# Performance work log

Hardware: AMD Instinct MI355X
Metric: run time of the kernel (lower is better)

## Reference

```python
import jax, jax.numpy as jnp
import numpy as np

N = 65536
DIMS = [512, 1000, 500, 250, 1]


def setup_inputs() -> dict:
    key = jax.random.key(0)
    ks = jax.random.split(key, 7)

    def init_w(k, fan_in, fan_out):
        return (jax.random.normal(k, (fan_in, fan_out), jnp.float32)
                / np.float32(np.sqrt(fan_in)))

    return {
        "repr_xy_hat": jax.random.normal(ks[0], (N, DIMS[0]), jnp.float32),
        "repr_xy": jax.random.normal(ks[1], (N, DIMS[0]), jnp.float32),
        "W1": init_w(ks[2], DIMS[0], DIMS[1]), "b1": jnp.zeros((DIMS[1],), jnp.float32),
        "W2": init_w(ks[3], DIMS[1], DIMS[2]), "b2": jnp.zeros((DIMS[2],), jnp.float32),
        "W3": init_w(ks[4], DIMS[2], DIMS[3]), "b3": jnp.zeros((DIMS[3],), jnp.float32),
        "W4": init_w(ks[5], DIMS[3], DIMS[4]), "b4": jnp.zeros((DIMS[4],), jnp.float32),
    }


def _disc_logits(x, W1, b1, W2, b2, W3, b3, W4, b4):
    # Batched version of the per-sample Linear-ReLU chain; sigmoid is folded
    # into the numerically stable BCE losses below.
    h = jax.nn.relu(x @ W1 + b1)
    h = jax.nn.relu(h @ W2 + b2)
    h = jax.nn.relu(h @ W3 + b3)
    return (h @ W4 + b4)[:, 0]  # [N]


def reference(repr_xy_hat, repr_xy, W1, b1, W2, b2, W3, b3, W4, b4):
    z_fake = _disc_logits(repr_xy_hat, W1, b1, W2, b2, W3, b3, W4, b4)  # [N]
    z_real = _disc_logits(repr_xy, W1, b1, W2, b2, W3, b3, W4, b4)      # [N]
    # generator loss: sum_i -log sigmoid(z_fake_i) = softplus(-z_fake)
    loss_F = jnp.sum(jax.nn.softplus(-z_fake))
    # discriminator loss: sum_i [-log sigmoid(z_real_i) - log(1 - sigmoid(z_fake_i))]
    # pred is detached in the original -> stop_gradient on the fake logits.
    z_fake_d = jax.lax.stop_gradient(z_fake)
    loss_D = jnp.sum(jax.nn.softplus(-z_real) + jax.nn.softplus(z_fake_d))
    return (loss_F, loss_D)
```

## Files before the change

### kernel.cpp

```cpp
#include <hip/hip_runtime.h>
#include <hip/hip_bf16.h>
#include <cmath>

using short4v = __attribute__((ext_vector_type(4))) short;
using f32x16  = __attribute__((ext_vector_type(16))) float;
using int8v   = __attribute__((ext_vector_type(8))) int;

#define MFMASC(a,b,c) __builtin_amdgcn_mfma_scale_f32_32x32x64_f8f6f4( \
    a, b, c, 0, 0, 0, 0x7F7F7F7F, 0, 0x7F7F7F7F)

__device__ __forceinline__ unsigned short f2bf(float f) {
    union { float f; unsigned u; } v; v.f = f;
    unsigned u = v.u;
    return (unsigned short)((u + 0x7FFFu + ((u >> 16) & 1u)) >> 16);
}
__device__ __forceinline__ float bf2f(unsigned short h) {
    union { unsigned u; float f; } v; v.u = ((unsigned)h) << 16;
    return v.f;
}
__device__ __forceinline__ float softplus(float x) {
    return fmaxf(x, 0.f) + log1pf(expf(-fabsf(x)));
}
__device__ __forceinline__ unsigned f4_to_fp8x4(float a, float b, float c, float d) {
    int v = __builtin_amdgcn_cvt_pk_fp8_f32(a, b, 0, false);
    v = __builtin_amdgcn_cvt_pk_fp8_f32(c, d, v, true);
    return (unsigned)v;
}
__device__ __forceinline__ int8v ld_a(const unsigned char* base, int o0, int o1) {
    int8v r;
    *((uint4*)&r)     = *(const uint4*)(base + o0);
    *((uint4*)&r + 1) = *(const uint4*)(base + o1);
    return r;
}
__device__ __forceinline__ int8v ld_w(const uint4* p) {
    int8v r;
    *((uint4*)&r)     = p[0];
    *((uint4*)&r + 1) = p[1];
    return r;
}

__global__ void pack_w_fp8g(const float* __restrict__ W, uint4* __restrict__ out,
                            int K_real, int M_real, int KG, int CT) {
    int tid = blockIdx.x * blockDim.x + threadIdx.x;
    if (tid >= CT * KG * 64) return;
    int lane = tid & 63;
    int t    = tid >> 6;
    int kg   = t % KG;
    int ct   = t / KG;
    int m  = ct * 32 + (lane & 31);
    int kb = kg * 64 + ((lane >> 5) << 5);
    float f[32];
#pragma unroll
    for (int j = 0; j < 32; ++j) {
        int k = kb + j;
        f[j] = (k < K_real && m < M_real) ? W[(size_t)k * M_real + m] : 0.f;
    }
    uint4 o0, o1;
    o0.x = f4_to_fp8x4(f[0],  f[1],  f[2],  f[3]);
    o0.y = f4_to_fp8x4(f[4],  f[5],  f[6],  f[7]);
    o0.z = f4_to_fp8x4(f[8],  f[9],  f[10], f[11]);
    o0.w = f4_to_fp8x4(f[12], f[13], f[14], f[15]);
    o1.x = f4_to_fp8x4(f[16], f[17], f[18], f[19]);
    o1.y = f4_to_fp8x4(f[20], f[21], f[22], f[23]);
    o1.z = f4_to_fp8x4(f[24], f[25], f[26], f[27]);
    o1.w = f4_to_fp8x4(f[28], f[29], f[30], f[31]);
    out[(size_t)tid * 2]     = o0;
    out[(size_t)tid * 2 + 1] = o1;
}

__global__ void pack_bias(const float* __restrict__ b1, const float* __restrict__ b2,
                          const float* __restrict__ b3, float* __restrict__ out) {
    int i = blockIdx.x * 256 + threadIdx.x;
    if (i < 1024)      out[i] = (i < 1000) ? b1[i] : 0.f;
    else if (i < 1536) { int j = i - 1024; out[i] = (j < 500) ? b2[j] : 0.f; }
    else if (i < 1792) { int j = i - 1536; out[i] = (j < 250) ? b3[j] : 0.f; }
}

__global__ __launch_bounds__(512, 4) void fused_mlp(
    const float* __restrict__ Xf, const float* __restrict__ Xr,
    const uint4* __restrict__ pW1, const uint4* __restrict__ pW2,
    const uint4* __restrict__ pW3, const float* __restrict__ biasp,
    const float* __restrict__ W4, const float* __restrict__ b4,
    float* __restrict__ partials)
{
    __shared__ __align__(16) unsigned char smem[66048];
    float* red = (float*)(smem + 65536);

    const int tidx = threadIdx.x;
    const int wid  = tidx >> 6;
    const int lane = tidx & 63;
    const int l31  = lane & 31;
    const int hi   = lane >> 5;
    const int swz  = (l31 & 15) << 4;

    const long grow0 = (long)blockIdx.x * 64;
    const float* X = (grow0 < 65536) ? (Xf + (size_t)grow0 * 512)
                                     : (Xr + (size_t)(grow0 - 65536) * 512);

#pragma unroll 1
    for (int gb = 0; gb < 4; ++gb) {
        float4 xr[4];
#pragma unroll
        for (int it = 0; it < 4; ++it) {
            int idx = (gb * 4 + it) * 512 + tidx;
            int r = idx >> 7; int k0 = (idx & 127) * 4;
            xr[it] = *(const float4*)(X + (size_t)r * 512 + k0);
        }
#pragma unroll
        for (int it = 0; it < 4; ++it) {
            int idx = (gb * 4 + it) * 512 + tidx;
            int r = idx >> 7; int k0 = (idx & 127) * 4;
            int pos = 512 + ((k0 & 0x1F0) ^ ((r & 15) << 4)) + (k0 & 12);
            *(unsigned*)(smem + r * 1024 + pos) =
                f4_to_fp8x4(xr[it].x, xr[it].y, xr[it].z, xr[it].w);
        }
    }
    __syncthreads();

#pragma unroll 1
    for (int p = 0; p < 2; ++p) {
        const uint4* wpA = pW1 + ((size_t)((p * 16 + wid * 2 + 0) * 8) * 64 + lane) * 2;
        const uint4* wpB = pW1 + ((size_t)((p * 16 + wid * 2 + 1) * 8) * 64 + lane) * 2;
        f32x16 acc[2][2];
#pragma unroll
        for (int c = 0; c < 2; ++c)
#pragma unroll
            for (int rt = 0; rt < 2; ++rt)
#pragma unroll
                for (int g = 0; g < 16; ++g) acc[c][rt][g] = 0.f;

#pragma unroll 1
        for (int kg = 0; kg < 8; ++kg) {
            int k0 = kg * 64 + hi * 32;
            const unsigned char* r0 = smem + l31 * 1024 + 512;
            const unsigned char* r1 = smem + (32 + l31) * 1024 + 512;
            int8v a0 = ld_a(r0, k0 ^ swz, (k0 + 16) ^ swz);
            int8v a1 = ld_a(r1, k0 ^ swz, (k0 + 16) ^ swz);
            int8v w0 = ld_w(wpA + (size_t)kg * 128);
            int8v w1 = ld_w(wpB + (size_t)kg * 128);
            acc[0][0] = MFMASC(w0, a0, acc[0][0]);
            acc[0][1] = MFMASC(w0, a1, acc[0][1]);
            acc[1][0] = MFMASC(w1, a0, acc[1][0]);
            acc[1][1] = MFMASC(w1, a1, acc[1][1]);
        }
        if (p == 1) __syncthreads();
#pragma unroll
        for (int c = 0; c < 2; ++c) {
            int mt = (p * 16 + wid * 2 + c) * 32;
#pragma unroll
            for (int rt = 0; rt < 2; ++rt) {
                int row = rt * 32 + l31;
#pragma unroll
                for (int q = 0; q < 4; ++q) {
                    int mg = mt + q * 8 + hi * 4;
                    float4 bb = *(const float4*)(biasp + mg);
                    float v0 = fmaxf(acc[c][rt][q * 4 + 0] + bb.x, 0.f);
                    float v1 = fmaxf(acc[c][rt][q * 4 + 1] + bb.y, 0.f);
                    float v2 = fmaxf(acc[c][rt][q * 4 + 2] + bb.z, 0.f);
                    float v3 = fmaxf(acc[c][rt][q * 4 + 3] + bb.w, 0.f);
                    *(unsigned*)(smem + row * 1024 + (mg ^ swz)) =
                        f4_to_fp8x4(v0, v1, v2, v3);
                }
            }
        }
    }
    __syncthreads();

    {
        const uint4* wpA = pW2 + ((size_t)((wid * 2 + 0) * 16) * 64 + lane) * 2;
        const uint4* wpB = pW2 + ((size_t)((wid * 2 + 1) * 16) * 64 + lane) * 2;
        f32x16 acc[2][2];
#pragma unroll
        for (int c = 0; c < 2; ++c)
#pragma unroll
            for (int rt = 0; rt < 2; ++rt)
#pragma unroll
                for (int g = 0; g < 16; ++g) acc[c][rt][g] = 0.f;
#pragma unroll 2
        for (int kg = 0; kg < 16; ++kg) {
            int k0 = kg * 64 + hi * 32;
            const unsigned char* r0 = smem + l31 * 1024;
            const unsigned char* r1 = smem + (32 + l31) * 1024;
            int8v a0 = ld_a(r0, k0 ^ swz, (k0 + 16) ^ swz);
            int8v a1 = ld_a(r1, k0 ^ swz, (k0 + 16) ^ swz);
            int8v w0 = ld_w(wpA + (size_t)kg * 128);
            int8v w1 = ld_w(wpB + (size_t)kg * 128);
            acc[0][0] = MFMASC(w0, a0, acc[0][0]);
            acc[0][1] = MFMASC(w0, a1, acc[0][1]);
            acc[1][0] = MFMASC(w1, a0, acc[1][0]);
            acc[1][1] = MFMASC(w1, a1, acc[1][1]);
        }
        __syncthreads();
#pragma unroll
        for (int c = 0; c < 2; ++c) {
            int mt = (wid * 2 + c) * 32;
#pragma unroll
            for (int rt = 0; rt < 2; ++rt) {
                int row = rt * 32 + l31;
#pragma unroll
                for (int q = 0; q < 4; ++q) {
                    int mg = mt + q * 8 + hi * 4;
                    float4 bb = *(const float4*)(biasp + 1024 + mg);
                    float v0 = fmaxf(acc[c][rt][q * 4 + 0] + bb.x, 0.f);
                    float v1 = fmaxf(acc[c][rt][q * 4 + 1] + bb.y, 0.f);
                    float v2 = fmaxf(acc[c][rt][q * 4 + 2] + bb.z, 0.f);
                    float v3 = fmaxf(acc[c][rt][q * 4 + 3] + bb.w, 0.f);
                    *(unsigned*)(smem + row * 512 + (mg ^ swz)) =
                        f4_to_fp8x4(v0, v1, v2, v3);
                }
            }
        }
    }
    __syncthreads();

    {
        const uint4* wp = pW3 + ((size_t)(wid * 8) * 64 + lane) * 2;
        f32x16 acc3[2];
#pragma unroll
        for (int rt = 0; rt < 2; ++rt)
#pragma unroll
            for (int g = 0; g < 16; ++g) acc3[rt][g] = 0.f;
#pragma unroll 1
        for (int kg = 0; kg < 8; ++kg) {
            int k0 = kg * 64 + hi * 32;
            const unsigned char* r0 = smem + l31 * 512;
            const unsigned char* r1 = smem + (32 + l31) * 512;
            int8v a0 = ld_a(r0, k0 ^ swz, (k0 + 16) ^ swz);
            int8v a1 = ld_a(r1, k0 ^ swz, (k0 + 16) ^ swz);
            int8v w = ld_w(wp + (size_t)kg * 128);
            acc3[0] = MFMASC(w, a0, acc3[0]);
            acc3[1] = MFMASC(w, a1, acc3[1]);
        }
        int mt = wid * 32;
#pragma unroll
        for (int rt = 0; rt < 2; ++rt) {
            int row = rt * 32 + l31;
#pragma unroll
            for (int q = 0; q < 4; ++q) {
                int mg = mt + q * 8 + hi * 4;
                float4 bb = *(const float4*)(biasp + 1536 + mg);
                short4v s;
                s[0] = (short)f2bf(fmaxf(acc3[rt][q * 4 + 0] + bb.x, 0.f));
                s[1] = (short)f2bf(fmaxf(acc3[rt][q * 4 + 1] + bb.y, 0.f));
                s[2] = (short)f2bf(fmaxf(acc3[rt][q * 4 + 2] + bb.z, 0.f));
                s[3] = (short)f2bf(fmaxf(acc3[rt][q * 4 + 3] + bb.w, 0.f));
                *(short4v*)(smem + 32768 + row * 512 + ((mg * 2) ^ swz)) = s;
            }
        }
    }
    __syncthreads();

    {
        int g  = tidx >> 3;
        int t8 = tidx & 7;
        int gs = (g & 15) << 4;
        float sum = 0.f;
#pragma unroll
        for (int o = 0; o < 4; ++o) {
            int colb = t8 * 32 + o * 8;
            short4v v0 = *(const short4v*)(smem + 32768 + g * 512 + ((colb * 2) ^ gs));
            short4v v1 = *(const short4v*)(smem + 32768 + g * 512 + ((colb * 2 + 8) ^ gs));
#pragma unroll
            for (int j = 0; j < 4; ++j) {
                int c0 = colb + j, c1 = colb + 4 + j;
                if (c0 < 250) sum += bf2f((unsigned short)v0[j]) * W4[c0];
                if (c1 < 250) sum += bf2f((unsigned short)v1[j]) * W4[c1];
            }
        }
        sum += __shfl_down(sum, 4, 8);
        sum += __shfl_down(sum, 2, 8);
        sum += __shfl_down(sum, 1, 8);
        if (t8 == 0) {
            float z = sum + b4[0];
            bool fake = (grow0 < 65536);
            float spn = softplus(-z);
            red[g]      = fake ? spn : 0.f;
            red[64 + g] = fake ? softplus(z) : spn;
        }
    }
    __syncthreads();
    if (tidx == 0) {
        float pF = 0.f, pD = 0.f;
        for (int i = 0; i < 64; ++i) { pF += red[i]; pD += red[64 + i]; }
        partials[(size_t)blockIdx.x * 2]     = pF;
        partials[(size_t)blockIdx.x * 2 + 1] = pD;
    }
}

__global__ void reduce_partials(const float* __restrict__ partials, int nblocks,
                                float* __restrict__ out) {
    __shared__ float sF[256], sD[256];
    float f = 0.f, d = 0.f;
    for (int i = threadIdx.x; i < nblocks; i += 256) {
        f += partials[2 * i];
        d += partials[2 * i + 1];
    }
    sF[threadIdx.x] = f; sD[threadIdx.x] = d;
    __syncthreads();
    for (int s = 128; s > 0; s >>= 1) {
        if (threadIdx.x < s) {
            sF[threadIdx.x] += sF[threadIdx.x + s];
            sD[threadIdx.x] += sD[threadIdx.x + s];
        }
        __syncthreads();
    }
    if (threadIdx.x == 0) { out[0] = sF[0]; out[1] = sD[0]; }
}

extern "C" void kernel_launch(void* const* d_in, const int* in_sizes, int n_in,
                              void* d_out, int out_size, void* d_ws, size_t ws_size,
                              hipStream_t stream) {
    const float* Xf = (const float*)d_in[0];
    const float* Xr = (const float*)d_in[1];
    const float* W1 = (const float*)d_in[2];
    const float* b1 = (const float*)d_in[3];
    const float* W2 = (const float*)d_in[4];
    const float* b2 = (const float*)d_in[5];
    const float* W3 = (const float*)d_in[6];
    const float* b3 = (const float*)d_in[7];
    const float* W4 = (const float*)d_in[8];
    const float* b4 = (const float*)d_in[9];

    uint4* pW1 = (uint4*)d_ws;
    uint4* pW2 = pW1 + 32768;
    uint4* pW3 = pW2 + 32768;
    float* biasp = (float*)(pW3 + 8192);
    float* partials = biasp + 2048;

    pack_w_fp8g<<<(32 * 8 * 64) / 256, 256, 0, stream>>>(W1, pW1, 512, 1000, 8, 32);
    pack_w_fp8g<<<(16 * 16 * 64) / 256, 256, 0, stream>>>(W2, pW2, 1000, 500, 16, 16);
    pack_w_fp8g<<<(8 * 8 * 64) / 256, 256, 0, stream>>>(W3, pW3, 500, 250, 8, 8);
    pack_bias<<<7, 256, 0, stream>>>(b1, b2, b3, biasp);

    fused_mlp<<<2048, 512, 0, stream>>>(Xf, Xr, pW1, pW2, pW3,
                                        biasp, W4, b4, partials);

    reduce_partials<<<1, 256, 0, stream>>>(partials, 2048, (float*)d_out);
}
```

Before: 194.1 us.

## Merge weight/bias packing into one launch and raise MFMA wave priority

```diff
diff --git a/kernel.cpp b/kernel.cpp
--- a/kernel.cpp
+++ b/kernel.cpp
@@ -39,10 +39,9 @@
     return r;
 }
 
-__global__ void pack_w_fp8g(const float* __restrict__ W, uint4* __restrict__ out,
-                            int K_real, int M_real, int KG, int CT) {
-    int tid = blockIdx.x * blockDim.x + threadIdx.x;
-    if (tid >= CT * KG * 64) return;
+__device__ __forceinline__ void pack_one(const float* __restrict__ W,
+                                         uint4* __restrict__ out,
+                                         int K_real, int M_real, int KG, int tid) {
     int lane = tid & 63;
     int t    = tid >> 6;
     int kg   = t % KG;
@@ -68,12 +67,24 @@
     out[(size_t)tid * 2 + 1] = o1;
 }
 
-__global__ void pack_bias(const float* __restrict__ b1, const float* __restrict__ b2,
-                          const float* __restrict__ b3, float* __restrict__ out) {
-    int i = blockIdx.x * 256 + threadIdx.x;
-    if (i < 1024)      out[i] = (i < 1000) ? b1[i] : 0.f;
-    else if (i < 1536) { int j = i - 1024; out[i] = (j < 500) ? b2[j] : 0.f; }
-    else if (i < 1792) { int j = i - 1536; out[i] = (j < 250) ? b3[j] : 0.f; }
+__global__ void prep_all(const float* __restrict__ W1, const float* __restrict__ W2,
+                         const float* __restrict__ W3, const float* __restrict__ b1,
+                         const float* __restrict__ b2, const float* __restrict__ b3,
+                         uint4* __restrict__ pW1, uint4* __restrict__ pW2,
+                         uint4* __restrict__ pW3, float* __restrict__ biasp) {
+    int tid = blockIdx.x * 256 + threadIdx.x;
+    if (tid < 16384) {
+        pack_one(W1, pW1, 512, 1000, 8, tid);
+    } else if (tid < 32768) {
+        pack_one(W2, pW2, 1000, 500, 16, tid - 16384);
+    } else if (tid < 36864) {
+        pack_one(W3, pW3, 500, 250, 8, tid - 32768);
+    } else if (tid < 38656) {
+        int i = tid - 36864;
+        if (i < 1024)      biasp[i] = (i < 1000) ? b1[i] : 0.f;
+        else if (i < 1536) { int j = i - 1024; biasp[i] = (j < 500) ? b2[j] : 0.f; }
+        else               { int j = i - 1536; biasp[i] = (j < 250) ? b3[j] : 0.f; }
+    }
 }
 
 __global__ __launch_bounds__(512, 4) void fused_mlp(
@@ -138,10 +149,12 @@
             int8v a1 = ld_a(r1, k0 ^ swz, (k0 + 16) ^ swz);
             int8v w0 = ld_w(wpA + (size_t)kg * 128);
             int8v w1 = ld_w(wpB + (size_t)kg * 128);
+            __builtin_amdgcn_s_setprio(1);
             acc[0][0] = MFMASC(w0, a0, acc[0][0]);
             acc[0][1] = MFMASC(w0, a1, acc[0][1]);
             acc[1][0] = MFMASC(w1, a0, acc[1][0]);
             acc[1][1] = MFMASC(w1, a1, acc[1][1]);
+            __builtin_amdgcn_s_setprio(0);
         }
         if (p == 1) __syncthreads();
 #pragma unroll
@@ -176,7 +189,7 @@
             for (int rt = 0; rt < 2; ++rt)
 #pragma unroll
                 for (int g = 0; g < 16; ++g) acc[c][rt][g] = 0.f;
-#pragma unroll 2
+#pragma unroll 1
         for (int kg = 0; kg < 16; ++kg) {
             int k0 = kg * 64 + hi * 32;
             const unsigned char* r0 = smem + l31 * 1024;
@@ -185,10 +198,12 @@
             int8v a1 = ld_a(r1, k0 ^ swz, (k0 + 16) ^ swz);
             int8v w0 = ld_w(wpA + (size_t)kg * 128);
             int8v w1 = ld_w(wpB + (size_t)kg * 128);
+            __builtin_amdgcn_s_setprio(1);
             acc[0][0] = MFMASC(w0, a0, acc[0][0]);
             acc[0][1] = MFMASC(w0, a1, acc[0][1]);
             acc[1][0] = MFMASC(w1, a0, acc[1][0]);
             acc[1][1] = MFMASC(w1, a1, acc[1][1]);
+            __builtin_amdgcn_s_setprio(0);
         }
         __syncthreads();
 #pragma unroll
@@ -228,8 +243,10 @@
             int8v a0 = ld_a(r0, k0 ^ swz, (k0 + 16) ^ swz);
             int8v a1 = ld_a(r1, k0 ^ swz, (k0 + 16) ^ swz);
             int8v w = ld_w(wp + (size_t)kg * 128);
+            __builtin_amdgcn_s_setprio(1);
             acc3[0] = MFMASC(w, a0, acc3[0]);
             acc3[1] = MFMASC(w, a1, acc3[1]);
+            __builtin_amdgcn_s_setprio(0);
         }
         int mt = wid * 32;
 #pragma unroll
@@ -327,10 +344,8 @@
     float* biasp = (float*)(pW3 + 8192);
     float* partials = biasp + 2048;
 
-    pack_w_fp8g<<<(32 * 8 * 64) / 256, 256, 0, stream>>>(W1, pW1, 512, 1000, 8, 32);
-    pack_w_fp8g<<<(16 * 16 * 64) / 256, 256, 0, stream>>>(W2, pW2, 1000, 500, 16, 16);
-    pack_w_fp8g<<<(8 * 8 * 64) / 256, 256, 0, stream>>>(W3, pW3, 500, 250, 8, 8);
-    pack_bias<<<7, 256, 0, stream>>>(b1, b2, b3, biasp);
+    prep_all<<<151, 256, 0, stream>>>(W1, W2, W3, b1, b2, b3,
+                                      pW1, pW2, pW3, biasp);
 
     fused_mlp<<<2048, 512, 0, stream>>>(Xf, Xr, pW1, pW2, pW3,
                                         biasp, W4, b4, partials);
```

After: 186.8 us. 3.8% less time.
